# Kernel optimization log

Hardware: AMD Instinct MI355X
Metric: run time of the kernel (lower is better)

The kernel has to match this reference:

```python
import jax, jax.numpy as jnp
import numpy as np
from jax import lax

DIM = 256
KS = 7
EPS = 1e-6


def setup_inputs() -> dict:
    key = jax.random.key(0)
    ks = jax.random.split(key, 10)
    x = jax.random.normal(ks[0], (32, DIM, 56, 56), dtype=jnp.float32)
    mask = jax.random.randint(ks[1], (32, 1, 7, 7), 0, 2, dtype=jnp.int32)
    dw_w = jax.random.normal(ks[2], (DIM, 1, KS, KS), dtype=jnp.float32) * (1.0 / KS)
    dw_b = jax.random.normal(ks[3], (DIM,), dtype=jnp.float32) * 0.01
    ln_w = jnp.ones((DIM,), dtype=jnp.float32)
    ln_b = jnp.zeros((DIM,), dtype=jnp.float32)
    w1 = jax.random.normal(ks[4], (DIM, 4 * DIM), dtype=jnp.float32) * (1.0 / np.sqrt(DIM))
    b1 = jax.random.normal(ks[5], (4 * DIM,), dtype=jnp.float32) * 0.01
    w2 = jax.random.normal(ks[6], (4 * DIM, DIM), dtype=jnp.float32) * (1.0 / np.sqrt(4 * DIM))
    b2 = jax.random.normal(ks[7], (DIM,), dtype=jnp.float32) * 0.01
    gamma = jnp.full((DIM,), 1e-6, dtype=jnp.float32)
    return {"x": x, "mask": mask, "dw_w": dw_w, "dw_b": dw_b, "ln_w": ln_w,
            "ln_b": ln_b, "w1": w1, "b1": b1, "w2": w2, "b2": b2, "gamma": gamma}


def _expand_mask(mask, H, W):
    # repeat_interleave the (B,1,f,f) mask up to (B,1,H,W)
    hr, wr = H // mask.shape[-2], W // mask.shape[-1]
    m = jnp.repeat(jnp.repeat(mask, hr, axis=2), wr, axis=3)
    return m


def reference(x, mask, dw_w, dw_b, ln_w, ln_b, w1, b1, w2, b2, gamma):
    B, C, H, W = x.shape
    m = _expand_mask(mask, H, W).astype(x.dtype)  # (B,1,H,W)
    inp = x
    # depthwise conv, 'same' padding
    pad = KS // 2
    y = lax.conv_general_dilated(
        x, dw_w, window_strides=(1, 1), padding=[(pad, pad), (pad, pad)],
        feature_group_count=C, dimension_numbers=("NCHW", "OIHW", "NCHW"))
    y = y + dw_b[None, :, None, None]
    y = y.transpose(0, 2, 3, 1)  # (B,H,W,C)
    # sparse LayerNorm: gather-norm-scatter == per-position LN zeroed at inactive
    mu = jnp.mean(y, axis=-1, keepdims=True)
    var = jnp.mean((y - mu) ** 2, axis=-1, keepdims=True)
    y = ((y - mu) * lax.rsqrt(var + EPS)) * ln_w + ln_b
    y = y * m[:, 0, :, :, None]
    # MLP
    h = jax.nn.gelu(jnp.einsum("bhwc,cd->bhwd", y, w1) + b1, approximate=False)
    z = (jnp.einsum("bhwd,dc->bhwc", h, w2) + b2) * gamma
    z = z.transpose(0, 3, 1, 2)  # (B,C,H,W)
    z = z * m
    return inp + z
```

## Files before the change

kernel.cpp:

```cpp
#include <hip/hip_runtime.h>
#include <math.h>

#define HW   56
#define DIMC 256
#define HID  1024

typedef __attribute__((ext_vector_type(8))) short bf16x8;
typedef __attribute__((ext_vector_type(4))) float f32x4;

__device__ __forceinline__ short f2bf(float f) {
  union { float fv; unsigned u; } v; v.fv = f;
  unsigned r = v.u + 0x7fffu + ((v.u >> 16) & 1u);
  return (short)(r >> 16);
}
__device__ __forceinline__ float bf2f(short s) {
  union { unsigned u; float fv; } v; v.u = ((unsigned)(unsigned short)s) << 16;
  return v.fv;
}
__device__ __forceinline__ float gelu_fast(float v) {
  float e = exp2f(-2.4556260f * v);
  return v * __builtin_amdgcn_rcpf(1.f + e);
}
__device__ __forceinline__ long pk8(float f0, float f1, float f2, float f3,
                                    float f4, float f5, float f6, float f7) {
  int lo = __builtin_amdgcn_cvt_pk_fp8_f32(f0, f1, 0, false);
  lo = __builtin_amdgcn_cvt_pk_fp8_f32(f2, f3, lo, true);
  int hi = __builtin_amdgcn_cvt_pk_fp8_f32(f4, f5, 0, false);
  hi = __builtin_amdgcn_cvt_pk_fp8_f32(f6, f7, hi, true);
  return ((long)(unsigned)lo) | ((long)hi << 32);
}
__device__ __forceinline__ char f2fp8(float f) {
  return (char)(__builtin_amdgcn_cvt_pk_fp8_f32(f, f, 0, false) & 0xff);
}

__global__ void prep_pack(const float* __restrict__ w1, const float* __restrict__ w2,
                          long* __restrict__ w1p, long* __restrict__ w2p) {
  int g = blockIdx.x * 256 + threadIdx.x;
  int f = g >> 6, lane = g & 63;
  int l15 = lane & 15, q = lane >> 4;
  float t[8];
  if (f < 512) {
    int k8 = f & 7, tt = f >> 3, nt = tt & 1, ch = tt >> 1;
    int n = ch * 32 + nt * 16 + l15;
    int k = k8 * 32 + q * 8;
    #pragma unroll
    for (int j = 0; j < 8; ++j) t[j] = w1[(k + j) * HID + n];
    w1p[f * 64 + lane] = pk8(t[0], t[1], t[2], t[3], t[4], t[5], t[6], t[7]);
  } else {
    int f2 = f - 512;
    int nt2 = f2 & 15, ch = f2 >> 4;
    int k = ch * 32 + q * 8;
    int c = nt2 * 16 + l15;
    #pragma unroll
    for (int j = 0; j < 8; ++j) t[j] = w2[(k + j) * DIMC + c];
    w2p[f2 * 64 + lane] = pk8(t[0], t[1], t[2], t[3], t[4], t[5], t[6], t[7]);
  }
}

__global__ __launch_bounds__(256, 3) void conv_k(
    const float* __restrict__ x, const int* __restrict__ mask,
    const float* __restrict__ dw_w, const float* __restrict__ dw_b,
    short* __restrict__ ybuf) {
  __shared__ __align__(16) float s_patch[32 * 14 * 20];
  __shared__ float s_wt[32 * 49];
  __shared__ __align__(16) short s_yout[32 * 64];

  int bid = blockIdx.x;
  int cgi = bid & 7; int t1 = bid >> 3;
  int wb = t1 % 7; int t2 = t1 / 7; int hb = t2 % 7; int b = t2 / 7;
  int tile = (b * 7 + hb) * 7 + wb;
  if (!mask[tile]) return;

  int tid = threadIdx.x;
  int h0 = hb * 8, w0 = wb * 8, cg0 = cgi * 32;

  for (int i = tid; i < 32 * 49; i += 256) s_wt[i] = dw_w[cg0 * 49 + i];

  #pragma unroll
  for (int it = 0; it < 7; ++it) {
    int slot = tid + 256 * it;
    int j = slot & 3, row = slot >> 2;
    int c = row / 14, r = row - c * 14;
    int gh = h0 - 3 + r;
    f32x4 v = (f32x4){0.f, 0.f, 0.f, 0.f};
    bool ok = (gh >= 0) && (gh < HW) && !(wb == 0 && j == 0) && !(wb == 6 && j == 3);
    if (ok)
      v = *(const f32x4*)(x + ((long)(b * DIMC + cg0 + c) * HW + gh) * HW + (w0 - 4) + 4 * j);
    *(f32x4*)(s_patch + c * 280 + r * 20 + 4 * j) = v;
  }
  __syncthreads();

  int cl = tid >> 3, wq = tid & 7;
  float wt[49];
  #pragma unroll
  for (int j = 0; j < 49; ++j) wt[j] = s_wt[cl * 49 + j];
  float y[8] = {0.f, 0.f, 0.f, 0.f, 0.f, 0.f, 0.f, 0.f};
  #pragma unroll
  for (int r = 0; r < 14; ++r) {
    float row[7];
    #pragma unroll
    for (int j = 0; j < 7; ++j) row[j] = s_patch[cl * 280 + r * 20 + wq + 1 + j];
    #pragma unroll
    for (int dy = 0; dy < 7; ++dy) {
      int hh = r - dy;
      if (hh >= 0 && hh < 8) {
        #pragma unroll
        for (int dx = 0; dx < 7; ++dx) y[hh] += row[dx] * wt[dy * 7 + dx];
      }
    }
  }
  float db = dw_b[cg0 + cl];
  #pragma unroll
  for (int hh = 0; hh < 8; ++hh)
    s_yout[cl * 64 + hh * 8 + wq] = f2bf(y[hh] + db);
  __syncthreads();

  int c = tid >> 3, pd = (tid & 7) * 8;
  bf16x8 v = *(const bf16x8*)(s_yout + c * 64 + pd);
  *(bf16x8*)(ybuf + ((long)tile * DIMC + cg0 + c) * 64 + pd) = v;
}

__global__ __launch_bounds__(256, 3) void mlp_k(
    const int* __restrict__ mask,
    const float* __restrict__ ln_w, const float* __restrict__ ln_b,
    const float* __restrict__ b1v, const float* __restrict__ b2v,
    const float* __restrict__ gammav,
    const long* __restrict__ w1p, const long* __restrict__ w2p,
    short* __restrict__ ybuf) {
  __shared__ __align__(16) char smem[46592];
  short* s_a   = (short*)smem;
  short* s_del = (short*)smem;
  char*  s_h8  = smem + 36864;
  float* s_p1  = (float*)(smem + 41984);
  float* s_p2  = (float*)(smem + 43008);
  float* s_mu  = (float*)(smem + 44032);
  float* s_rs  = (float*)(smem + 44288);
  float* s_lnw = (float*)(smem + 44544);
  float* s_lnb = (float*)(smem + 45568);

  int tile = blockIdx.x;
  if (!mask[tile]) return;
  int tid = threadIdx.x;
  const short* ytile = ybuf + (long)tile * DIMC * 64;

  s_lnw[tid] = ln_w[tid];
  s_lnb[tid] = ln_b[tid];
  #pragma unroll
  for (int k = 0; k < 8; ++k) {
    int q4 = tid + 256 * k;
    int c = q4 & 255, pd = (q4 >> 8) * 8;
    bf16x8 v = *(const bf16x8*)(ytile + c * 64 + pd);
    #pragma unroll
    for (int j = 0; j < 8; ++j) s_a[(pd + j) * 264 + c] = v[j];
  }
  __syncthreads();

  {
    int p = tid & 63, cq = tid >> 6;
    bf16x8 va[8];
    float s1 = 0.f, s2 = 0.f;
    #pragma unroll
    for (int i = 0; i < 8; ++i) {
      va[i] = *(const bf16x8*)(s_a + p * 264 + cq * 64 + i * 8);
      #pragma unroll
      for (int j = 0; j < 8; ++j) {
        float f = bf2f(va[i][j]);
        s1 += f; s2 += f * f;
      }
    }
    s_p1[cq * 64 + p] = s1; s_p2[cq * 64 + p] = s2;
    __syncthreads();
    if (tid < 64) {
      float t1 = s_p1[tid] + s_p1[64 + tid] + s_p1[128 + tid] + s_p1[192 + tid];
      float t2 = s_p2[tid] + s_p2[64 + tid] + s_p2[128 + tid] + s_p2[192 + tid];
      float mu = t1 * (1.f / 256.f);
      float var = t2 * (1.f / 256.f) - mu * mu;
      s_mu[tid] = mu; s_rs[tid] = rsqrtf(var + 1e-6f);
    }
    __syncthreads();
    float mu = s_mu[p], rs = s_rs[p];
    #pragma unroll
    for (int i = 0; i < 8; ++i) {
      int c0 = cq * 64 + i * 8;
      bf16x8 v = va[i];
      #pragma unroll
      for (int j = 0; j < 8; ++j)
        v[j] = f2bf((bf2f(v[j]) - mu) * rs * s_lnw[c0 + j] + s_lnb[c0 + j]);
      *(bf16x8*)(s_a + p * 264 + c0) = v;
    }
  }
  __syncthreads();

  const int wv = tid >> 6, lane = tid & 63;
  const int l15 = lane & 15, q = lane >> 4;
  const int mh = wv & 1, nh = wv >> 1;

  const short* aRow0 = s_a + (32 * mh + l15) * 264 + q * 8;
  const short* aRow1 = s_a + (32 * mh + 16 + l15) * 264 + q * 8;
  long a0f[8], a1f[8];
  #pragma unroll
  for (int k8 = 0; k8 < 8; ++k8) {
    bf16x8 v0 = *(const bf16x8*)(aRow0 + k8 * 32);
    bf16x8 v1 = *(const bf16x8*)(aRow1 + k8 * 32);
    a0f[k8] = pk8(bf2f(v0[0]), bf2f(v0[1]), bf2f(v0[2]), bf2f(v0[3]),
                  bf2f(v0[4]), bf2f(v0[5]), bf2f(v0[6]), bf2f(v0[7]));
    a1f[k8] = pk8(bf2f(v1[0]), bf2f(v1[1]), bf2f(v1[2]), bf2f(v1[3]),
                  bf2f(v1[4]), bf2f(v1[5]), bf2f(v1[6]), bf2f(v1[7]));
  }

  f32x4 z[4][4];
  #pragma unroll
  for (int jt = 0; jt < 4; ++jt)
    #pragma unroll
    for (int Mt = 0; Mt < 4; ++Mt) z[jt][Mt] = (f32x4){0.f, 0.f, 0.f, 0.f};

  long w1r[8];
  #pragma unroll
  for (int k8 = 0; k8 < 8; ++k8)
    w1r[k8] = w1p[(long)(nh * 8 + k8) * 64 + lane];

  for (int ch = 0; ch < 32; ++ch) {
    long w2r[4];
    #pragma unroll
    for (int jt = 0; jt < 4; ++jt)
      w2r[jt] = w2p[(long)(ch * 16 + wv * 4 + jt) * 64 + lane];
    float bb = b1v[ch * 32 + 16 * nh + l15];

    f32x4 acc0 = (f32x4){0.f, 0.f, 0.f, 0.f};
    f32x4 acc1 = (f32x4){0.f, 0.f, 0.f, 0.f};
    __builtin_amdgcn_s_setprio(1);
    #pragma unroll
    for (int k8 = 0; k8 < 8; ++k8) {
      acc0 = __builtin_amdgcn_mfma_f32_16x16x32_fp8_fp8(a0f[k8], w1r[k8], acc0, 0, 0, 0);
      acc1 = __builtin_amdgcn_mfma_f32_16x16x32_fp8_fp8(a1f[k8], w1r[k8], acc1, 0, 0, 0);
    }
    __builtin_amdgcn_s_setprio(0);
    long w1n[8];
    if (ch < 31) {
      #pragma unroll
      for (int k8 = 0; k8 < 8; ++k8)
        w1n[k8] = w1p[(long)(((ch + 1) * 2 + nh) * 8 + k8) * 64 + lane];
    }
    char* hb = s_h8 + (ch & 1) * 2560;
    #pragma unroll
    for (int r = 0; r < 4; ++r) {
      hb[(32 * mh + 4 * q + r) * 40 + 16 * nh + l15]      = f2fp8(gelu_fast(acc0[r] + bb));
      hb[(32 * mh + 16 + 4 * q + r) * 40 + 16 * nh + l15] = f2fp8(gelu_fast(acc1[r] + bb));
    }
    __syncthreads();
    __builtin_amdgcn_s_setprio(1);
    #pragma unroll
    for (int Mt = 0; Mt < 4; ++Mt) {
      long aH = *(const long*)(hb + (16 * Mt + l15) * 40 + q * 8);
      #pragma unroll
      for (int jt = 0; jt < 4; ++jt)
        z[jt][Mt] = __builtin_amdgcn_mfma_f32_16x16x32_fp8_fp8(aH, w2r[jt], z[jt][Mt], 0, 0, 0);
    }
    __builtin_amdgcn_s_setprio(0);
    if (ch < 31) {
      #pragma unroll
      for (int k8 = 0; k8 < 8; ++k8) w1r[k8] = w1n[k8];
    }
  }

  #pragma unroll
  for (int jt = 0; jt < 4; ++jt) {
    int c = wv * 64 + jt * 16 + l15;
    float bb = b2v[c], gm = gammav[c];
    #pragma unroll
    for (int Mt = 0; Mt < 4; ++Mt) {
      #pragma unroll
      for (int r = 0; r < 4; ++r)
        s_del[c * 72 + 16 * Mt + 4 * q + r] = f2bf((z[jt][Mt][r] + bb) * gm);
    }
  }
  __syncthreads();
  short* dtile = ybuf + (long)tile * DIMC * 64;
  #pragma unroll
  for (int k = 0; k < 8; ++k) {
    int q4 = tid + 256 * k;
    int c = q4 & 255, pd = (q4 >> 8) * 8;
    bf16x8 v = *(const bf16x8*)(s_del + c * 72 + pd);
    *(bf16x8*)(dtile + c * 64 + pd) = v;
  }
}

__global__ __launch_bounds__(256) void epi_k(
    const float* __restrict__ x, const int* __restrict__ mask,
    const short* __restrict__ delta, float* __restrict__ out) {
  const int NU = 32 * DIMC * HW * 7;
  int stride = gridDim.x * 256;
  for (int u = blockIdx.x * 256 + threadIdx.x; u < NU; u += stride) {
    int wb = u % 7; int t1 = u / 7;
    int h = t1 % 56; int t2 = t1 / 56;
    int c = t2 & 255; int b = t2 >> 8;
    int g = ((b * DIMC + c) * HW + h) * HW + wb * 8;
    f32x4 x0 = *(const f32x4*)(x + g);
    f32x4 x1 = *(const f32x4*)(x + g + 4);
    int tile = (b * 7 + (h >> 3)) * 7 + wb;
    if (mask[tile]) {
      bf16x8 d = *(const bf16x8*)(delta + ((long)tile * DIMC + c) * 64 + (h & 7) * 8);
      #pragma unroll
      for (int i = 0; i < 4; ++i) { x0[i] += bf2f(d[i]); x1[i] += bf2f(d[4 + i]); }
    }
    *(f32x4*)(out + g) = x0;
    *(f32x4*)(out + g + 4) = x1;
  }
}

extern "C" void kernel_launch(void* const* d_in, const int* in_sizes, int n_in,
                              void* d_out, int out_size, void* d_ws, size_t ws_size,
                              hipStream_t stream) {
  const float* x    = (const float*)d_in[0];
  const int*   mask = (const int*)d_in[1];
  const float* dw_w = (const float*)d_in[2];
  const float* dw_b = (const float*)d_in[3];
  const float* ln_w = (const float*)d_in[4];
  const float* ln_b = (const float*)d_in[5];
  const float* w1   = (const float*)d_in[6];
  const float* b1   = (const float*)d_in[7];
  const float* w2   = (const float*)d_in[8];
  const float* b2   = (const float*)d_in[9];
  const float* gm   = (const float*)d_in[10];
  float* out = (float*)d_out;

  long* w1p  = (long*)d_ws;
  long* w2p  = w1p + 512 * 64;
  short* ybuf = (short*)(w2p + 512 * 64);

  prep_pack<<<256, 256, 0, stream>>>(w1, w2, w1p, w2p);
  conv_k<<<12544, 256, 0, stream>>>(x, mask, dw_w, dw_b, ybuf);
  mlp_k<<<1568, 256, 0, stream>>>(mask, ln_w, ln_b, b1, b2, gm, w1p, w2p, ybuf);
  epi_k<<<4096, 256, 0, stream>>>(x, mask, ybuf, out);
}
```

Measured before the change: 372.7 us.

## Shrink conv and MLP shared memory, store delta as fp8, apply gamma in epilogue

The conv kernel now handles 16 channels per block with 4 output rows per thread, loads weights straight from global memory and reuses the patch buffer for output, which cuts LDS use and doubles the grid. The MLP kernel reads bf16 activations directly from global memory for LayerNorm and writes the normalized values to LDS as fp8, roughly halving its shared memory. This lets both kernels declare 4 blocks per CU. The MLP delta is stored as fp8 without the gamma scale, and the epilogue applies gamma while reading half as many bytes, at some precision risk from the fp8 residual.

```diff
diff --git a/kernel.cpp b/kernel.cpp
--- a/kernel.cpp
+++ b/kernel.cpp
@@ -57,237 +57,226 @@
   }
 }
 
-__global__ __launch_bounds__(256, 3) void conv_k(
+__global__ __launch_bounds__(256, 4) void conv_k(
     const float* __restrict__ x, const int* __restrict__ mask,
     const float* __restrict__ dw_w, const float* __restrict__ dw_b,
     short* __restrict__ ybuf) {
-  __shared__ __align__(16) float s_patch[32 * 14 * 20];
-  __shared__ float s_wt[32 * 49];
-  __shared__ __align__(16) short s_yout[32 * 64];
+  __shared__ __align__(16) float s_patch[16 * 14 * 20];
+  short* s_yout = (short*)s_patch;
 
   int bid = blockIdx.x;
-  int cgi = bid & 7; int t1 = bid >> 3;
+  int cgi = bid & 15; int t1 = bid >> 4;
   int wb = t1 % 7; int t2 = t1 / 7; int hb = t2 % 7; int b = t2 / 7;
   int tile = (b * 7 + hb) * 7 + wb;
   if (!mask[tile]) return;
 
   int tid = threadIdx.x;
-  int h0 = hb * 8, w0 = wb * 8, cg0 = cgi * 32;
-
-  for (int i = tid; i < 32 * 49; i += 256) s_wt[i] = dw_w[cg0 * 49 + i];
-
-  #pragma unroll
-  for (int it = 0; it < 7; ++it) {
+  int h0 = hb * 8, w0 = wb * 8, cg0 = cgi * 16;
+
+  #pragma unroll
+  for (int it = 0; it < 4; ++it) {
     int slot = tid + 256 * it;
-    int j = slot & 3, row = slot >> 2;
-    int c = row / 14, r = row - c * 14;
-    int gh = h0 - 3 + r;
-    f32x4 v = (f32x4){0.f, 0.f, 0.f, 0.f};
-    bool ok = (gh >= 0) && (gh < HW) && !(wb == 0 && j == 0) && !(wb == 6 && j == 3);
-    if (ok)
-      v = *(const f32x4*)(x + ((long)(b * DIMC + cg0 + c) * HW + gh) * HW + (w0 - 4) + 4 * j);
-    *(f32x4*)(s_patch + c * 280 + r * 20 + 4 * j) = v;
-  }
-  __syncthreads();
-
-  int cl = tid >> 3, wq = tid & 7;
+    if (slot < 896) {
+      int j = slot & 3, row = slot >> 2;
+      int c = row / 14, r = row - c * 14;
+      int gh = h0 - 3 + r;
+      f32x4 v = (f32x4){0.f, 0.f, 0.f, 0.f};
+      bool ok = (gh >= 0) && (gh < HW) && !(wb == 0 && j == 0) && !(wb == 6 && j == 3);
+      if (ok)
+        v = *(const f32x4*)(x + ((long)(b * DIMC + cg0 + c) * HW + gh) * HW + (w0 - 4) + 4 * j);
+      *(f32x4*)(s_patch + c * 280 + r * 20 + 4 * j) = v;
+    }
+  }
+
+  int cl = tid >> 4, s = tid & 15;
+  int wq = s & 7, hf = s >> 3;
   float wt[49];
   #pragma unroll
-  for (int j = 0; j < 49; ++j) wt[j] = s_wt[cl * 49 + j];
-  float y[8] = {0.f, 0.f, 0.f, 0.f, 0.f, 0.f, 0.f, 0.f};
-  #pragma unroll
-  for (int r = 0; r < 14; ++r) {
+  for (int j = 0; j < 49; ++j) wt[j] = dw_w[(cg0 + cl) * 49 + j];
+  __syncthreads();
+
+  float y[4] = {0.f, 0.f, 0.f, 0.f};
+  #pragma unroll
+  for (int rr = 0; rr < 10; ++rr) {
     float row[7];
     #pragma unroll
-    for (int j = 0; j < 7; ++j) row[j] = s_patch[cl * 280 + r * 20 + wq + 1 + j];
+    for (int j = 0; j < 7; ++j) row[j] = s_patch[cl * 280 + (hf * 4 + rr) * 20 + wq + 1 + j];
     #pragma unroll
     for (int dy = 0; dy < 7; ++dy) {
-      int hh = r - dy;
-      if (hh >= 0 && hh < 8) {
+      int hh = rr - dy;
+      if (hh >= 0 && hh < 4) {
         #pragma unroll
         for (int dx = 0; dx < 7; ++dx) y[hh] += row[dx] * wt[dy * 7 + dx];
       }
     }
   }
   float db = dw_b[cg0 + cl];
-  #pragma unroll
-  for (int hh = 0; hh < 8; ++hh)
-    s_yout[cl * 64 + hh * 8 + wq] = f2bf(y[hh] + db);
-  __syncthreads();
-
-  int c = tid >> 3, pd = (tid & 7) * 8;
-  bf16x8 v = *(const bf16x8*)(s_yout + c * 64 + pd);
-  *(bf16x8*)(ybuf + ((long)tile * DIMC + cg0 + c) * 64 + pd) = v;
-}
-
-__global__ __launch_bounds__(256, 3) void mlp_k(
+  __syncthreads();
+  #pragma unroll
+  for (int hh = 0; hh < 4; ++hh)
+    s_yout[cl * 64 + (hf * 4 + hh) * 8 + wq] = f2bf(y[hh] + db);
+  __syncthreads();
+
+  if (tid < 128) {
+    int c = tid >> 3, pd = (tid & 7) * 8;
+    bf16x8 v = *(const bf16x8*)(s_yout + c * 64 + pd);
+    *(bf16x8*)(ybuf + ((long)tile * DIMC + cg0 + c) * 64 + pd) = v;
+  }
+}
+
+__global__ __launch_bounds__(256, 4) void mlp_k(
     const int* __restrict__ mask,
     const float* __restrict__ ln_w, const float* __restrict__ ln_b,
     const float* __restrict__ b1v, const float* __restrict__ b2v,
-    const float* __restrict__ gammav,
     const long* __restrict__ w1p, const long* __restrict__ w2p,
     short* __restrict__ ybuf) {
-  __shared__ __align__(16) char smem[46592];
-  short* s_a   = (short*)smem;
-  short* s_del = (short*)smem;
-  char*  s_h8  = smem + 36864;
-  float* s_p1  = (float*)(smem + 41984);
-  float* s_p2  = (float*)(smem + 43008);
-  float* s_mu  = (float*)(smem + 44032);
-  float* s_rs  = (float*)(smem + 44288);
-  float* s_lnw = (float*)(smem + 44544);
-  float* s_lnb = (float*)(smem + 45568);
+  __shared__ __align__(16) char smem[28160];
+  char*  s_a8  = smem;
+  char*  s_del8 = smem;
+  char*  s_h8  = smem + 18432;
+  float* s_p1  = (float*)(smem + 23552);
+  float* s_p2  = (float*)(smem + 24576);
+  float* s_mu  = (float*)(smem + 25600);
+  float* s_rs  = (float*)(smem + 25856);
+  float* s_lnw = (float*)(smem + 26112);
+  float* s_lnb = (float*)(smem + 27136);
 
   int tile = blockIdx.x;
   if (!mask[tile]) return;
   int tid = threadIdx.x;
-  const short* ytile = ybuf + (long)tile * DIMC * 64;
+  const unsigned short* ytile = (const unsigned short*)(ybuf + (long)tile * DIMC * 64);
 
   s_lnw[tid] = ln_w[tid];
   s_lnb[tid] = ln_b[tid];
+
+  int p = tid & 63, cq = tid >> 6;
+  {
+    float s1 = 0.f, s2 = 0.f;
+    #pragma unroll 8
+    for (int i = 0; i < 64; ++i) {
+      float f = bf2f((short)ytile[(cq * 64 + i) * 64 + p]);
+      s1 += f; s2 += f * f;
+    }
+    s_p1[cq * 64 + p] = s1; s_p2[cq * 64 + p] = s2;
+  }
+  __syncthreads();
+  if (tid < 64) {
+    float t1 = s_p1[tid] + s_p1[64 + tid] + s_p1[128 + tid] + s_p1[192 + tid];
+    float t2 = s_p2[tid] + s_p2[64 + tid] + s_p2[128 + tid] + s_p2[192 + tid];
+    float mu = t1 * (1.f / 256.f);
+    float var = t2 * (1.f / 256.f) - mu * mu;
+    s_mu[tid] = mu; s_rs[tid] = rsqrtf(var + 1e-6f);
+  }
+  __syncthreads();
+  {
+    float mu = s_mu[p], rs = s_rs[p];
+    #pragma unroll
+    for (int i = 0; i < 8; ++i) {
+      int c0 = cq * 64 + i * 8;
+      float f[8];
+      #pragma unroll
+      for (int j = 0; j < 8; ++j) {
+        float v = bf2f((short)ytile[(c0 + j) * 64 + p]);
+        f[j] = (v - mu) * rs * s_lnw[c0 + j] + s_lnb[c0 + j];
+      }
+      *(long*)(s_a8 + p * 280 + c0) = pk8(f[0], f[1], f[2], f[3], f[4], f[5], f[6], f[7]);
+    }
+  }
+  __syncthreads();
+
+  const int wv = tid >> 6, lane = tid & 63;
+  const int l15 = lane & 15, q = lane >> 4;
+  const int mh = wv & 1, nh = wv >> 1;
+
+  long a0f[8], a1f[8];
+  #pragma unroll
+  for (int k8 = 0; k8 < 8; ++k8) {
+    a0f[k8] = *(const long*)(s_a8 + (32 * mh + l15) * 280 + k8 * 32 + q * 8);
+    a1f[k8] = *(const long*)(s_a8 + (32 * mh + 16 + l15) * 280 + k8 * 32 + q * 8);
+  }
+
+  f32x4 z[4][4];
+  #pragma unroll
+  for (int jt = 0; jt < 4; ++jt)
+    #pragma unroll
+    for (int Mt = 0; Mt < 4; ++Mt) z[jt][Mt] = (f32x4){0.f, 0.f, 0.f, 0.f};
+
+  long w1r[8];
+  #pragma unroll
+  for (int k8 = 0; k8 < 8; ++k8)
+    w1r[k8] = w1p[(long)(nh * 8 + k8) * 64 + lane];
+
+  for (int ch = 0; ch < 32; ++ch) {
+    long w2r[4];
+    #pragma unroll
+    for (int jt = 0; jt < 4; ++jt)
+      w2r[jt] = w2p[(long)(ch * 16 + wv * 4 + jt) * 64 + lane];
+    float bb = b1v[ch * 32 + 16 * nh + l15];
+
+    f32x4 acc0 = (f32x4){0.f, 0.f, 0.f, 0.f};
+    f32x4 acc1 = (f32x4){0.f, 0.f, 0.f, 0.f};
+    __builtin_amdgcn_s_setprio(1);
+    #pragma unroll
+    for (int k8 = 0; k8 < 8; ++k8) {
+      acc0 = __builtin_amdgcn_mfma_f32_16x16x32_fp8_fp8(a0f[k8], w1r[k8], acc0, 0, 0, 0);
+      acc1 = __builtin_amdgcn_mfma_f32_16x16x32_fp8_fp8(a1f[k8], w1r[k8], acc1, 0, 0, 0);
+    }
+    __builtin_amdgcn_s_setprio(0);
+    long w1n[8];
+    if (ch < 31) {
+      #pragma unroll
+      for (int k8 = 0; k8 < 8; ++k8)
+        w1n[k8] = w1p[(long)(((ch + 1) * 2 + nh) * 8 + k8) * 64 + lane];
+    }
+    char* hb = s_h8 + (ch & 1) * 2560;
+    #pragma unroll
+    for (int r = 0; r < 4; ++r) {
+      hb[(32 * mh + 4 * q + r) * 40 + 16 * nh + l15]      = f2fp8(gelu_fast(acc0[r] + bb));
+      hb[(32 * mh + 16 + 4 * q + r) * 40 + 16 * nh + l15] = f2fp8(gelu_fast(acc1[r] + bb));
+    }
+    __syncthreads();
+    __builtin_amdgcn_s_setprio(1);
+    #pragma unroll
+    for (int Mt = 0; Mt < 4; ++Mt) {
+      long aH = *(const long*)(hb + (16 * Mt + l15) * 40 + q * 8);
+      #pragma unroll
+      for (int jt = 0; jt < 4; ++jt)
+        z[jt][Mt] = __builtin_amdgcn_mfma_f32_16x16x32_fp8_fp8(aH, w2r[jt], z[jt][Mt], 0, 0, 0);
+    }
+    __builtin_amdgcn_s_setprio(0);
+    if (ch < 31) {
+      #pragma unroll
+      for (int k8 = 0; k8 < 8; ++k8) w1r[k8] = w1n[k8];
+    }
+  }
+
+  #pragma unroll
+  for (int jt = 0; jt < 4; ++jt) {
+    int c = wv * 64 + jt * 16 + l15;
+    float bb = b2v[c];
+    #pragma unroll
+    for (int Mt = 0; Mt < 4; ++Mt) {
+      #pragma unroll
+      for (int r = 0; r < 4; ++r)
+        s_del8[c * 72 + 16 * Mt + 4 * q + r] = f2fp8(z[jt][Mt][r] + bb);
+    }
+  }
+  __syncthreads();
+  char* dtile8 = (char*)(ybuf + (long)tile * DIMC * 64);
   #pragma unroll
   for (int k = 0; k < 8; ++k) {
     int q4 = tid + 256 * k;
     int c = q4 & 255, pd = (q4 >> 8) * 8;
-    bf16x8 v = *(const bf16x8*)(ytile + c * 64 + pd);
-    #pragma unroll
-    for (int j = 0; j < 8; ++j) s_a[(pd + j) * 264 + c] = v[j];
-  }
-  __syncthreads();
-
-  {
-    int p = tid & 63, cq = tid >> 6;
-    bf16x8 va[8];
-    float s1 = 0.f, s2 = 0.f;
-    #pragma unroll
-    for (int i = 0; i < 8; ++i) {
-      va[i] = *(const bf16x8*)(s_a + p * 264 + cq * 64 + i * 8);
-      #pragma unroll
-      for (int j = 0; j < 8; ++j) {
-        float f = bf2f(va[i][j]);
-        s1 += f; s2 += f * f;
-      }
-    }
-    s_p1[cq * 64 + p] = s1; s_p2[cq * 64 + p] = s2;
-    __syncthreads();
-    if (tid < 64) {
-      float t1 = s_p1[tid] + s_p1[64 + tid] + s_p1[128 + tid] + s_p1[192 + tid];
-      float t2 = s_p2[tid] + s_p2[64 + tid] + s_p2[128 + tid] + s_p2[192 + tid];
-      float mu = t1 * (1.f / 256.f);
-      float var = t2 * (1.f / 256.f) - mu * mu;
-      s_mu[tid] = mu; s_rs[tid] = rsqrtf(var + 1e-6f);
-    }
-    __syncthreads();
-    float mu = s_mu[p], rs = s_rs[p];
-    #pragma unroll
-    for (int i = 0; i < 8; ++i) {
-      int c0 = cq * 64 + i * 8;
-      bf16x8 v = va[i];
-      #pragma unroll
-      for (int j = 0; j < 8; ++j)
-        v[j] = f2bf((bf2f(v[j]) - mu) * rs * s_lnw[c0 + j] + s_lnb[c0 + j]);
-      *(bf16x8*)(s_a + p * 264 + c0) = v;
-    }
-  }
-  __syncthreads();
-
-  const int wv = tid >> 6, lane = tid & 63;
-  const int l15 = lane & 15, q = lane >> 4;
-  const int mh = wv & 1, nh = wv >> 1;
-
-  const short* aRow0 = s_a + (32 * mh + l15) * 264 + q * 8;
-  const short* aRow1 = s_a + (32 * mh + 16 + l15) * 264 + q * 8;
-  long a0f[8], a1f[8];
-  #pragma unroll
-  for (int k8 = 0; k8 < 8; ++k8) {
-    bf16x8 v0 = *(const bf16x8*)(aRow0 + k8 * 32);
-    bf16x8 v1 = *(const bf16x8*)(aRow1 + k8 * 32);
-    a0f[k8] = pk8(bf2f(v0[0]), bf2f(v0[1]), bf2f(v0[2]), bf2f(v0[3]),
-                  bf2f(v0[4]), bf2f(v0[5]), bf2f(v0[6]), bf2f(v0[7]));
-    a1f[k8] = pk8(bf2f(v1[0]), bf2f(v1[1]), bf2f(v1[2]), bf2f(v1[3]),
-                  bf2f(v1[4]), bf2f(v1[5]), bf2f(v1[6]), bf2f(v1[7]));
-  }
-
-  f32x4 z[4][4];
-  #pragma unroll
-  for (int jt = 0; jt < 4; ++jt)
-    #pragma unroll
-    for (int Mt = 0; Mt < 4; ++Mt) z[jt][Mt] = (f32x4){0.f, 0.f, 0.f, 0.f};
-
-  long w1r[8];
-  #pragma unroll
-  for (int k8 = 0; k8 < 8; ++k8)
-    w1r[k8] = w1p[(long)(nh * 8 + k8) * 64 + lane];
-
-  for (int ch = 0; ch < 32; ++ch) {
-    long w2r[4];
-    #pragma unroll
-    for (int jt = 0; jt < 4; ++jt)
-      w2r[jt] = w2p[(long)(ch * 16 + wv * 4 + jt) * 64 + lane];
-    float bb = b1v[ch * 32 + 16 * nh + l15];
-
-    f32x4 acc0 = (f32x4){0.f, 0.f, 0.f, 0.f};
-    f32x4 acc1 = (f32x4){0.f, 0.f, 0.f, 0.f};
-    __builtin_amdgcn_s_setprio(1);
-    #pragma unroll
-    for (int k8 = 0; k8 < 8; ++k8) {
-      acc0 = __builtin_amdgcn_mfma_f32_16x16x32_fp8_fp8(a0f[k8], w1r[k8], acc0, 0, 0, 0);
-      acc1 = __builtin_amdgcn_mfma_f32_16x16x32_fp8_fp8(a1f[k8], w1r[k8], acc1, 0, 0, 0);
-    }
-    __builtin_amdgcn_s_setprio(0);
-    long w1n[8];
-    if (ch < 31) {
-      #pragma unroll
-      for (int k8 = 0; k8 < 8; ++k8)
-        w1n[k8] = w1p[(long)(((ch + 1) * 2 + nh) * 8 + k8) * 64 + lane];
-    }
-    char* hb = s_h8 + (ch & 1) * 2560;
-    #pragma unroll
-    for (int r = 0; r < 4; ++r) {
-      hb[(32 * mh + 4 * q + r) * 40 + 16 * nh + l15]      = f2fp8(gelu_fast(acc0[r] + bb));
-      hb[(32 * mh + 16 + 4 * q + r) * 40 + 16 * nh + l15] = f2fp8(gelu_fast(acc1[r] + bb));
-    }
-    __syncthreads();
-    __builtin_amdgcn_s_setprio(1);
-    #pragma unroll
-    for (int Mt = 0; Mt < 4; ++Mt) {
-      long aH = *(const long*)(hb + (16 * Mt + l15) * 40 + q * 8);
-      #pragma unroll
-      for (int jt = 0; jt < 4; ++jt)
-        z[jt][Mt] = __builtin_amdgcn_mfma_f32_16x16x32_fp8_fp8(aH, w2r[jt], z[jt][Mt], 0, 0, 0);
-    }
-    __builtin_amdgcn_s_setprio(0);
-    if (ch < 31) {
-      #pragma unroll
-      for (int k8 = 0; k8 < 8; ++k8) w1r[k8] = w1n[k8];
-    }
-  }
-
-  #pragma unroll
-  for (int jt = 0; jt < 4; ++jt) {
-    int c = wv * 64 + jt * 16 + l15;
-    float bb = b2v[c], gm = gammav[c];
-    #pragma unroll
-    for (int Mt = 0; Mt < 4; ++Mt) {
-      #pragma unroll
-      for (int r = 0; r < 4; ++r)
-        s_del[c * 72 + 16 * Mt + 4 * q + r] = f2bf((z[jt][Mt][r] + bb) * gm);
-    }
-  }
-  __syncthreads();
-  short* dtile = ybuf + (long)tile * DIMC * 64;
-  #pragma unroll
-  for (int k = 0; k < 8; ++k) {
-    int q4 = tid + 256 * k;
-    int c = q4 & 255, pd = (q4 >> 8) * 8;
-    bf16x8 v = *(const bf16x8*)(s_del + c * 72 + pd);
-    *(bf16x8*)(dtile + c * 64 + pd) = v;
+    long v = *(const long*)(s_del8 + c * 72 + pd);
+    *(long*)(dtile8 + c * 64 + pd) = v;
   }
 }
 
 __global__ __launch_bounds__(256) void epi_k(
     const float* __restrict__ x, const int* __restrict__ mask,
-    const short* __restrict__ delta, float* __restrict__ out) {
+    const short* __restrict__ delta, const float* __restrict__ gammav,
+    float* __restrict__ out) {
+  const char* delta8 = (const char*)delta;
   const int NU = 32 * DIMC * HW * 7;
   int stride = gridDim.x * 256;
   for (int u = blockIdx.x * 256 + threadIdx.x; u < NU; u += stride) {
@@ -299,9 +288,17 @@
     f32x4 x1 = *(const f32x4*)(x + g + 4);
     int tile = (b * 7 + (h >> 3)) * 7 + wb;
     if (mask[tile]) {
-      bf16x8 d = *(const bf16x8*)(delta + ((long)tile * DIMC + c) * 64 + (h & 7) * 8);
-      #pragma unroll
-      for (int i = 0; i < 4; ++i) { x0[i] += bf2f(d[i]); x1[i] += bf2f(d[4 + i]); }
+      long dl = *(const long*)(delta8 + (long)tile * 32768 + c * 64 + (h & 7) * 8);
+      int lo = (int)(unsigned)dl, hi = (int)((unsigned long)dl >> 32);
+      float gm = gammav[c];
+      x0[0] += gm * __builtin_amdgcn_cvt_f32_fp8(lo, 0);
+      x0[1] += gm * __builtin_amdgcn_cvt_f32_fp8(lo, 1);
+      x0[2] += gm * __builtin_amdgcn_cvt_f32_fp8(lo, 2);
+      x0[3] += gm * __builtin_amdgcn_cvt_f32_fp8(lo, 3);
+      x1[0] += gm * __builtin_amdgcn_cvt_f32_fp8(hi, 0);
+      x1[1] += gm * __builtin_amdgcn_cvt_f32_fp8(hi, 1);
+      x1[2] += gm * __builtin_amdgcn_cvt_f32_fp8(hi, 2);
+      x1[3] += gm * __builtin_amdgcn_cvt_f32_fp8(hi, 3);
     }
     *(f32x4*)(out + g) = x0;
     *(f32x4*)(out + g + 4) = x1;
@@ -329,7 +326,7 @@
   short* ybuf = (short*)(w2p + 512 * 64);
 
   prep_pack<<<256, 256, 0, stream>>>(w1, w2, w1p, w2p);
-  conv_k<<<12544, 256, 0, stream>>>(x, mask, dw_w, dw_b, ybuf);
-  mlp_k<<<1568, 256, 0, stream>>>(mask, ln_w, ln_b, b1, b2, gm, w1p, w2p, ybuf);
-  epi_k<<<4096, 256, 0, stream>>>(x, mask, ybuf, out);
-}
+  conv_k<<<25088, 256, 0, stream>>>(x, mask, dw_w, dw_b, ybuf);
+  mlp_k<<<1568, 256, 0, stream>>>(mask, ln_w, ln_b, b1, b2, w1p, w2p, ybuf);
+  epi_k<<<4096, 256, 0, stream>>>(x, mask, ybuf, gm, out);
+}
```

Result: slower. 412.2 us (+10.6%).
